# Kernel optimization log

Hardware: AMD Instinct MI355X
Metric: run time of the kernel (lower is better)

The kernel has to match this reference:

```python
import jax, jax.numpy as jnp
import numpy as np

EPS = 1e-5

def _conv3x3(x, w, b):
    # NCHW, OIHW, 3x3 stride 1 pad 1
    y = jax.lax.conv_general_dilated(x, w, window_strides=(1, 1),
                                     padding=((1, 1), (1, 1)),
                                     dimension_numbers=('NCHW', 'OIHW', 'NCHW'))
    return y + b[None, :, None, None]

def _pool_upsample(x, k):
    # adaptive avg pool to (H/k, W/k) then nearest block-upsample back
    B, C, H, W = x.shape
    p = x.reshape(B, C, H // k, k, W // k, k).mean(axis=(3, 5))
    return jnp.repeat(jnp.repeat(p, k, axis=2), k, axis=3)

def setup_inputs() -> dict:
    key = jax.random.key(0)
    ks = jax.random.split(key, 12)
    B, C, H, W = 32, 8, 300, 300
    d = {
        'x': jax.random.normal(ks[0], (B, C, H, W), jnp.float32),
        'w5': jax.random.normal(ks[1], (8, 16, 3, 3), jnp.float32) * 0.1,
        'b5': jnp.zeros((8,), jnp.float32),
        'w10': jax.random.normal(ks[2], (8, 16, 3, 3), jnp.float32) * 0.1,
        'b10': jnp.zeros((8,), jnp.float32),
        'w15': jax.random.normal(ks[3], (8, 16, 3, 3), jnp.float32) * 0.1,
        'b15': jnp.zeros((8,), jnp.float32),
        'gw': jax.random.normal(ks[4], (8, 24, 3, 3), jnp.float32) * 0.1,
        'gb': jnp.zeros((8,), jnp.float32),
        'mw': jax.random.normal(ks[5], (8, 24, 3, 3), jnp.float32) * 0.1,
        'mb': jnp.zeros((8,), jnp.float32),
        'gamma': jnp.ones((8,), jnp.float32),
        'beta': jnp.zeros((8,), jnp.float32),
    }
    return d

def reference(x, w5, b5, w10, b10, w15, b15, gw, gb, mw, mb, gamma, beta):
    up5 = _pool_upsample(x, 5)    # [B,8,300,300]
    up10 = _pool_upsample(x, 10)
    up15 = _pool_upsample(x, 15)
    c5 = _conv3x3(jnp.concatenate([x, up5], axis=1), w5, b5)
    c10 = _conv3x3(jnp.concatenate([x, up10], axis=1), w10, b10)
    c15 = _conv3x3(jnp.concatenate([x, up15], axis=1), w15, b15)
    g_in = jnp.concatenate([c5, c10, c15], axis=1)  # [B,24,H,W]
    # gated conv, activation=None: conv(g_in) * sigmoid(mask_conv(g_in))
    y = _conv3x3(g_in, gw, gb) * jax.nn.sigmoid(_conv3x3(g_in, mw, mb))
    # batch norm (training-mode batch stats, biased var, as torch default)
    mean = y.mean(axis=(0, 2, 3), keepdims=True)
    var = ((y - mean) ** 2).mean(axis=(0, 2, 3), keepdims=True)
    y = (y - mean) * jax.lax.rsqrt(var + EPS)
    return y * gamma[None, :, None, None] + beta[None, :, None, None]
```

## Files before the change

### kernel.cpp

```cpp
#include <hip/hip_runtime.h>
#include <math.h>

typedef __bf16 bfrag __attribute__((ext_vector_type(8)));
typedef __bf16 bf16x4 __attribute__((ext_vector_type(4)));
typedef __bf16 bf16x8 __attribute__((ext_vector_type(8)));
typedef float f32x4 __attribute__((ext_vector_type(4)));

#define BN 32
#define HH 300
#define WW 300
#define HW 90000
#define NPX (BN * HW)

#define GX 10
#define GY 19

#define P5I_BYTE_OFF   0
#define P10I_BYTE_OFF  1843200
#define P15I_BYTE_OFF  2304000
#define CWB_BYTE_OFF   2508800
#define GWB_BYTE_OFF   2524160
#define STAT_BYTE_OFF  2531328
#define SS_BYTE_OFF    2539520
#define XBF_BYTE_OFF   2539584
#define XBF_END        (XBF_BYTE_OFF + (size_t)NPX * 16)

__device__ __forceinline__ short f2bf(float f) {
    union { float f; unsigned u; } v;
    v.f = f;
    unsigned r = v.u + 0x7FFF + ((v.u >> 16) & 1);
    return (short)(r >> 16);
}

__device__ __forceinline__ float bf2f(unsigned short s) {
    union { unsigned u; float f; } v;
    v.u = ((unsigned)s) << 16;
    return v.f;
}

__global__ void k_setup(const float* __restrict__ w5, const float* __restrict__ w10,
                        const float* __restrict__ w15, const float* __restrict__ gw,
                        const float* __restrict__ mw, short* __restrict__ cBg,
                        short* __restrict__ gBg, double* __restrict__ stats) {
    int t = threadIdx.x;
    for (int idx = t; idx < 7680; idx += 256) {
        int s = idx / 2560, rem = idx % 2560;
        int n = rem / 160, r2 = rem % 160;
        int tap = r2 / 16, ci = r2 % 16;
        float v = 0.f;
        if (n < 8 && tap < 9) {
            const float* W = (s == 0) ? w5 : ((s == 1) ? w10 : w15);
            v = W[(n * 16 + ci) * 9 + tap];
        }
        cBg[idx] = f2bf(v);
    }
    for (int idx = t; idx < 3584; idx += 256) {
        int n = idx / 224, r2 = idx % 224;
        int blk = r2 / 8, cj = r2 % 8;
        float v = 0.f;
        if (blk < 27) {
            int tap = blk / 3, ci24 = (blk % 3) * 8 + cj;
            if (n < 8) v = gw[(n * 24 + ci24) * 9 + tap];
            else       v = mw[((n - 8) * 24 + ci24) * 9 + tap];
        }
        gBg[idx] = f2bf(v);
    }
    for (int idx = t; idx < 16 * 64; idx += 256) stats[idx] = 0.0;
}

__global__ void k_pool5(const float* __restrict__ x, unsigned short* __restrict__ p5i) {
    int id = blockIdx.x * 256 + threadIdx.x;
    int bc = id / 3600, cell = id % 3600;
    int b = bc >> 3, c = bc & 7;
    int pi = cell / 60, pj = cell % 60;
    const float* rp = x + (size_t)bc * HW + pi * 5 * WW + pj * 5;
    float s = 0.f;
#pragma unroll
    for (int u = 0; u < 5; u++)
#pragma unroll
        for (int v = 0; v < 5; v++) s += rp[u * WW + v];
    p5i[((size_t)b * 3600 + cell) * 8 + c] = (unsigned short)f2bf(s * 0.04f);
}

__global__ __launch_bounds__(256) void k_prep(const float* __restrict__ x,
                                              unsigned short* __restrict__ xbf,
                                              unsigned short* __restrict__ p5i) {
    __shared__ float tf[8][5][304];
    const int t = threadIdx.x;
    const int pi = blockIdx.x, b = blockIdx.y;
    for (int idx = t; idx < 3000; idx += 256) {
        int ch = idx / 375, rem = idx % 375;
        int r = rem / 75, j = rem % 75;
        float4 v = *(const float4*)&x[((size_t)(b * 8 + ch) * HH + pi * 5 + r) * WW + 4 * j];
        *(float4*)&tf[ch][r][4 * j] = v;
    }
    __syncthreads();
    for (int idx = t; idx < 1500; idx += 256) {
        int r = idx / 300, c = idx - r * 300;
        bf16x8 pk;
#pragma unroll
        for (int ch = 0; ch < 8; ch++) pk[ch] = (__bf16)tf[ch][r][c];
        *(bf16x8*)&xbf[((size_t)b * HW + (pi * 5 + r) * WW + c) * 8] = pk;
    }
    for (int idx = t; idx < 512; idx += 256) {
        int ch = idx >> 6, pj = idx & 63;
        if (pj < 60) {
            float s = 0.f;
#pragma unroll
            for (int u = 0; u < 5; u++)
#pragma unroll
                for (int v = 0; v < 5; v++) s += tf[ch][u][pj * 5 + v];
            p5i[((size_t)b * 3600 + pi * 60 + pj) * 8 + ch] = (unsigned short)f2bf(s * 0.04f);
        }
    }
}

__global__ void k_poolD(const unsigned short* __restrict__ p5i,
                        unsigned short* __restrict__ p10i,
                        unsigned short* __restrict__ p15i) {
    int id = blockIdx.x * 256 + threadIdx.x;
    if (id < 230400) {
        int bc = id / 900, cell = id % 900;
        int b = bc >> 3, c = bc & 7;
        int pi = cell / 30, pj = cell % 30;
        const unsigned short* base = p5i + ((size_t)b * 3600) * 8 + c;
        float s = bf2f(base[((2 * pi) * 60 + 2 * pj) * 8]) +
                  bf2f(base[((2 * pi) * 60 + 2 * pj + 1) * 8]) +
                  bf2f(base[((2 * pi + 1) * 60 + 2 * pj) * 8]) +
                  bf2f(base[((2 * pi + 1) * 60 + 2 * pj + 1) * 8]);
        p10i[((size_t)b * 900 + cell) * 8 + c] = (unsigned short)f2bf(s * 0.25f);
    } else if (id < 332800) {
        int id2 = id - 230400;
        int bc = id2 / 400, cell = id2 % 400;
        int b = bc >> 3, c = bc & 7;
        int pi = cell / 20, pj = cell % 20;
        const unsigned short* base = p5i + ((size_t)b * 3600) * 8 + c;
        float s = 0.f;
#pragma unroll
        for (int u = 0; u < 3; u++)
#pragma unroll
            for (int v = 0; v < 3; v++)
                s += bf2f(base[((3 * pi + u) * 60 + 3 * pj + v) * 8]);
        p15i[((size_t)b * 400 + cell) * 8 + c] = (unsigned short)f2bf(s * (1.f / 9.f));
    }
}

template <int K, int PW>
__device__ __forceinline__ void up_load(const unsigned short* __restrict__ pooled,
                                        int b, int r0, int c0, int t, uint4* v) {
#pragma unroll
    for (int it = 0; it < 3; it++) {
        int idx = t + 256 * it;
        uint4 val = {0u, 0u, 0u, 0u};
        if (idx < 720) {
            int i = idx / 36, j = idx - i * 36;
            int ra = r0 - 2 + i, ca = c0 - 2 + j;
            if (ra >= 0 && ra < HH && ca >= 0 && ca < WW) {
                int pi = (int)((unsigned)ra / K);
                int pj = (int)((unsigned)ca / K);
                val = *(const uint4*)&pooled[((size_t)b * (PW * PW) + pi * PW + pj) * 8];
            }
        }
        v[it] = val;
    }
}

__device__ __forceinline__ void up_store(short* xuU, int t, const uint4* v) {
#pragma unroll
    for (int it = 0; it < 3; it++) {
        int idx = t + 256 * it;
        if (idx < 720) *(uint4*)&xuU[idx * 8] = v[it];
    }
}

__device__ __forceinline__ void c_phase(const short* xuX, const short* xuU,
                                        short* cwS,
                                        const unsigned short* __restrict__ cBs,
                                        const float* __restrict__ bias, int s,
                                        int r0, int c0, int lane, int wid, bool edge) {
    const int n = lane & 15, quad = lane >> 4;
    const int qh = quad >> 1, ql = quad & 1;
    const short* xbase = ql ? xuU : xuX;
    bfrag wfr[5];
    int dpoff[5];
#pragma unroll
    for (int km = 0; km < 5; km++) {
        int tapw = km * 2 + qh;
        int tapa = (tapw > 8) ? 8 : tapw;
        wfr[km] = *(const bfrag*)&cBs[(n * 10 + tapw) * 16 + ql * 8];
        dpoff[km] = ((tapa / 3) * 36 + tapa % 3) * 8;
    }
    float bO[4];
#pragma unroll
    for (int r = 0; r < 4; r++) bO[r] = bias[(quad & 1) * 4 + r];

    for (int g = wid; g < 39; g += 4) {
        int px = g * 16 + n;
        if (px > 611) px = 611;
        int rp = (int)((unsigned)px / 34u);
        int cp = px - rp * 34;
        int pb = (rp * 36 + cp) * 8;
        f32x4 acc = {0.f, 0.f, 0.f, 0.f};
#pragma unroll
        for (int km = 0; km < 5; km++)
            acc = __builtin_amdgcn_mfma_f32_16x16x32_bf16(
                wfr[km], *(const bfrag*)&xbase[pb + dpoff[km]], acc, 0, 0, 0);
        if (quad < 2) {
            bf16x4 pk;
#pragma unroll
            for (int r = 0; r < 4; r++) pk[r] = (__bf16)(acc[r] + bO[r]);
            if (edge) {
                int ra = r0 - 1 + rp, ca = c0 - 1 + cp;
                if (ra < 0 || ra >= HH || ca < 0 || ca >= WW) {
#pragma unroll
                    for (int r = 0; r < 4; r++) pk[r] = (__bf16)0.f;
                }
            }
            *(bf16x4*)&cwS[px * 24 + s * 8 + quad * 4] = pk;
        }
    }
}

template <bool XBF>
__global__ __launch_bounds__(256, 3) void k_fused(
    const float* __restrict__ x, const unsigned short* __restrict__ xbf,
    const unsigned short* __restrict__ p5i, const unsigned short* __restrict__ p10i,
    const unsigned short* __restrict__ p15i,
    const unsigned short* __restrict__ cBg, const unsigned short* __restrict__ gBg,
    const float* __restrict__ b5, const float* __restrict__ b10, const float* __restrict__ b15,
    const float* __restrict__ gb, const float* __restrict__ mb,
    float* __restrict__ out, double* __restrict__ stats) {
    __shared__ __align__(16) short xuX[720 * 8];
    __shared__ __align__(16) short xuU[720 * 8];
    __shared__ __align__(16) short cwS[612 * 24];

    const int b = blockIdx.z;
    const int r0 = blockIdx.y * 16, c0 = blockIdx.x * 32;
    const int t = threadIdx.x, lane = t & 63, wid = t >> 6;
    const bool edge = (blockIdx.x == 0) | (blockIdx.x == GX - 1) |
                      (blockIdx.y == 0) | (blockIdx.y == GY - 1);

    uint4 upv[3];
    up_load<5, 60>(p5i, b, r0, c0, t, upv);

    if constexpr (XBF) {
        for (int it = 0; it < 3; it++) {
            int idx = t + 256 * it;
            if (idx < 720) {
                int i = idx / 36, j = idx - i * 36;
                int ra = r0 - 2 + i, ca = c0 - 2 + j;
                uint4 v = {0u, 0u, 0u, 0u};
                if (ra >= 0 && ra < HH && ca >= 0 && ca < WW)
                    v = *(const uint4*)&xbf[((size_t)b * HW + ra * WW + ca) * 8];
                *(uint4*)&xuX[idx * 8] = v;
            }
        }
    } else {
        for (int idx = t; idx < 1440; idx += 256) {
            int cp = idx / 360, rem = idx % 360;
            int i = rem / 18, jp = rem % 18;
            int j = 2 * jp;
            int ra = r0 - 2 + i, ca = c0 - 2 + j;
            float2 v0 = {0.f, 0.f}, v1 = {0.f, 0.f};
            if (ra >= 0 && ra < HH && ca >= 0 && ca <= WW - 2) {
                size_t base = ((size_t)(b * 8 + 2 * cp) * HH + ra) * WW + ca;
                v0 = *(const float2*)&x[base];
                v1 = *(const float2*)&x[base + HW];
            }
            unsigned pA = (unsigned short)f2bf(v0.x) | ((unsigned)(unsigned short)f2bf(v1.x) << 16);
            unsigned pB = (unsigned short)f2bf(v0.y) | ((unsigned)(unsigned short)f2bf(v1.y) << 16);
            int px = i * 36 + j;
            *(unsigned*)&xuX[px * 8 + 2 * cp] = pA;
            *(unsigned*)&xuX[(px + 1) * 8 + 2 * cp] = pB;
        }
    }
    up_store(xuU, t, upv);
    __syncthreads();

    c_phase(xuX, xuU, cwS, cBg, b5, 0, r0, c0, lane, wid, edge);
    up_load<10, 30>(p10i, b, r0, c0, t, upv);
    __syncthreads();
    up_store(xuU, t, upv);
    __syncthreads();

    c_phase(xuX, xuU, cwS, cBg + 2560, b10, 1, r0, c0, lane, wid, edge);
    up_load<15, 20>(p15i, b, r0, c0, t, upv);
    __syncthreads();
    up_store(xuU, t, upv);
    __syncthreads();

    c_phase(xuX, xuU, cwS, cBg + 5120, b15, 2, r0, c0, lane, wid, edge);
    __syncthreads();

    const int n = lane & 15, quad = lane >> 4;
    bfrag gfr[7];
    int goff[7];
#pragma unroll
    for (int km = 0; km < 7; km++) {
        int blkw = km * 4 + quad;
        int blka = (blkw > 26) ? 26 : blkw;
        gfr[km] = *(const bfrag*)&gBg[(n * 28 + blkw) * 8];
        int tap = blka / 3, cig = blka - tap * 3;
        goff[km] = ((tap / 3) * 34 + tap % 3) * 24 + cig * 8;
    }
    float gO[4], mO[4];
#pragma unroll
    for (int r = 0; r < 4; r++) {
        gO[r] = gb[(quad & 1) * 4 + r];
        mO[r] = mb[(quad & 1) * 4 + r];
    }
    float ls[4] = {0.f, 0.f, 0.f, 0.f}, ls2[4] = {0.f, 0.f, 0.f, 0.f};

    for (int g = wid; g < 32; g += 4) {
        int px = g * 16 + n;
        int rr = px >> 5, cc = px & 31;
        int off0 = (rr * 34 + cc) * 24;
        f32x4 acc = {0.f, 0.f, 0.f, 0.f};
#pragma unroll
        for (int km = 0; km < 7; km++)
            acc = __builtin_amdgcn_mfma_f32_16x16x32_bf16(
                gfr[km], *(const bfrag*)&cwS[off0 + goff[km]], acc, 0, 0, 0);
        int ra = r0 + rr, ca = c0 + cc;
        bool wr = !edge || (ra < HH && ca < WW);
#pragma unroll
        for (int reg = 0; reg < 4; reg++) {
            float other = __shfl_xor(acc[reg], 32);
            if (quad < 2 && wr) {
                float G = acc[reg] + gO[reg];
                float M = other + mO[reg];
                float y = G * __builtin_amdgcn_rcpf(1.f + __expf(-M));
                int ch = quad * 4 + reg;
                out[(size_t)(b * 8 + ch) * HW + ra * WW + ca] = y;
                ls[reg] += y;
                ls2[reg] += y * y;
            }
        }
    }
#pragma unroll
    for (int m = 1; m < 16; m <<= 1) {
#pragma unroll
        for (int r = 0; r < 4; r++) {
            ls[r] += __shfl_xor(ls[r], m);
            ls2[r] += __shfl_xor(ls2[r], m);
        }
    }
    if (n == 0 && quad < 2) {
        int hash = (blockIdx.x + GX * blockIdx.y + GX * GY * blockIdx.z) & 63;
#pragma unroll
        for (int r = 0; r < 4; r++) {
            atomicAdd(&stats[(quad * 4 + r) * 64 + hash], (double)ls[r]);
            atomicAdd(&stats[(8 + quad * 4 + r) * 64 + hash], (double)ls2[r]);
        }
    }
}

__global__ void k_stats(const double* __restrict__ stats, const float* __restrict__ gamma,
                        const float* __restrict__ beta, float* __restrict__ ss) {
    __shared__ double tot[16];
    int t = threadIdx.x;
    if (t < 16) {
        double s = 0.0;
        for (int i = 0; i < 64; i++) s += stats[t * 64 + i];
        tot[t] = s;
    }
    __syncthreads();
    if (t < 8) {
        double N = (double)NPX;
        double mean = tot[t] / N;
        double var = tot[8 + t] / N - mean * mean;
        double scale = (double)gamma[t] / sqrt(var + 1e-5);
        ss[t] = (float)scale;
        ss[8 + t] = (float)((double)beta[t] - mean * scale);
    }
}

__global__ void k_norm(float* __restrict__ out, const float* __restrict__ ss) {
    int i = blockIdx.x * 256 + threadIdx.x;
    if (i < (BN * 8 * HW) / 4) {
        int plane = (i * 4) / HW;
        int ch = plane & 7;
        float sc = ss[ch], sh = ss[8 + ch];
        float4* p = (float4*)out + i;
        float4 v = *p;
        v.x = v.x * sc + sh;
        v.y = v.y * sc + sh;
        v.z = v.z * sc + sh;
        v.w = v.w * sc + sh;
        *p = v;
    }
}

extern "C" void kernel_launch(void* const* d_in, const int* in_sizes, int n_in,
                              void* d_out, int out_size, void* d_ws, size_t ws_size,
                              hipStream_t stream) {
    const float* x = (const float*)d_in[0];
    const float* w5 = (const float*)d_in[1];
    const float* b5 = (const float*)d_in[2];
    const float* w10 = (const float*)d_in[3];
    const float* b10 = (const float*)d_in[4];
    const float* w15 = (const float*)d_in[5];
    const float* b15 = (const float*)d_in[6];
    const float* gw = (const float*)d_in[7];
    const float* gb = (const float*)d_in[8];
    const float* mw = (const float*)d_in[9];
    const float* mb = (const float*)d_in[10];
    const float* gamma = (const float*)d_in[11];
    const float* beta = (const float*)d_in[12];

    float* out = (float*)d_out;
    unsigned short* p5i = (unsigned short*)((char*)d_ws + P5I_BYTE_OFF);
    unsigned short* p10i = (unsigned short*)((char*)d_ws + P10I_BYTE_OFF);
    unsigned short* p15i = (unsigned short*)((char*)d_ws + P15I_BYTE_OFF);
    short* cBg = (short*)((char*)d_ws + CWB_BYTE_OFF);
    short* gBg = (short*)((char*)d_ws + GWB_BYTE_OFF);
    double* stats = (double*)((char*)d_ws + STAT_BYTE_OFF);
    float* ss = (float*)((char*)d_ws + SS_BYTE_OFF);
    unsigned short* xbf = (unsigned short*)((char*)d_ws + XBF_BYTE_OFF);

    const bool use_xbf = (ws_size >= XBF_END);

    k_setup<<<1, 256, 0, stream>>>(w5, w10, w15, gw, mw, cBg, gBg, stats);
    if (use_xbf) {
        k_prep<<<dim3(60, 32), 256, 0, stream>>>(x, xbf, p5i);
    } else {
        k_pool5<<<3600, 256, 0, stream>>>(x, p5i);
    }
    k_poolD<<<1300, 256, 0, stream>>>(p5i, p10i, p15i);
    dim3 grid(GX, GY, BN);
    if (use_xbf) {
        k_fused<true><<<grid, 256, 0, stream>>>(x, xbf, p5i, p10i, p15i,
                                                (const unsigned short*)cBg, (const unsigned short*)gBg,
                                                b5, b10, b15, gb, mb, out, stats);
    } else {
        k_fused<false><<<grid, 256, 0, stream>>>(x, xbf, p5i, p10i, p15i,
                                                 (const unsigned short*)cBg, (const unsigned short*)gBg,
                                                 b5, b10, b15, gb, mb, out, stats);
    }
    k_stats<<<1, 64, 0, stream>>>(stats, gamma, beta, ss);
    k_norm<<<(BN * 8 * HW / 4 + 255) / 256, 256, 0, stream>>>(out, ss);
}
```

Baseline: 390.7 us.

## Split prep into xbf conversion and pool kernels, planar conv LDS layout

Replaces the fused prep kernel with a simple per-pixel fp32-to-bf16 channel-interleave kernel that also performs weight setup, removing one launch. A separate kernel then computes 5x5 pooling from the bf16 buffer. The intermediate conv outputs in LDS move from an interleaved 24-channel layout to three planar 8-channel buffers, which is meant to cut bank conflicts. The gated epilogue now splits the sigmoid and gate work across half-waves before the shuffle, and the stats reduction is parallelized. Pooling from bf16 instead of fp32 changes rounding slightly and adds an extra read pass over xbf.

```diff
diff --git a/kernel.cpp b/kernel.cpp
--- a/kernel.cpp
+++ b/kernel.cpp
@@ -14,6 +14,9 @@
 
 #define GX 10
 #define GY 19
+#define CPX 612
+#define XPX 720
+#define CWSTRIDE 4896
 
 #define P5I_BYTE_OFF   0
 #define P10I_BYTE_OFF  1843200
@@ -38,12 +41,16 @@
     return v.f;
 }
 
-__global__ void k_setup(const float* __restrict__ w5, const float* __restrict__ w10,
-                        const float* __restrict__ w15, const float* __restrict__ gw,
-                        const float* __restrict__ mw, short* __restrict__ cBg,
-                        short* __restrict__ gBg, double* __restrict__ stats) {
-    int t = threadIdx.x;
-    for (int idx = t; idx < 7680; idx += 256) {
+__device__ __forceinline__ void setup_body(int gid, int gstride,
+                                           const float* __restrict__ w5,
+                                           const float* __restrict__ w10,
+                                           const float* __restrict__ w15,
+                                           const float* __restrict__ gw,
+                                           const float* __restrict__ mw,
+                                           short* __restrict__ cBg,
+                                           short* __restrict__ gBg,
+                                           double* __restrict__ stats) {
+    for (int idx = gid; idx < 7680; idx += gstride) {
         int s = idx / 2560, rem = idx % 2560;
         int n = rem / 160, r2 = rem % 160;
         int tap = r2 / 16, ci = r2 % 16;
@@ -54,7 +61,7 @@
         }
         cBg[idx] = f2bf(v);
     }
-    for (int idx = t; idx < 3584; idx += 256) {
+    for (int idx = gid; idx < 3584; idx += gstride) {
         int n = idx / 224, r2 = idx % 224;
         int blk = r2 / 8, cj = r2 % 8;
         float v = 0.f;
@@ -65,7 +72,39 @@
         }
         gBg[idx] = f2bf(v);
     }
-    for (int idx = t; idx < 16 * 64; idx += 256) stats[idx] = 0.0;
+    for (int idx = gid; idx < 16 * 64; idx += gstride) stats[idx] = 0.0;
+}
+
+__global__ void k_setup(const float* __restrict__ w5, const float* __restrict__ w10,
+                        const float* __restrict__ w15, const float* __restrict__ gw,
+                        const float* __restrict__ mw, short* __restrict__ cBg,
+                        short* __restrict__ gBg, double* __restrict__ stats) {
+    setup_body(threadIdx.x, 256, w5, w10, w15, gw, mw, cBg, gBg, stats);
+}
+
+__global__ __launch_bounds__(256) void k_xbf(const float* __restrict__ x,
+                                             unsigned short* __restrict__ xbf,
+                                             const float* __restrict__ w5,
+                                             const float* __restrict__ w10,
+                                             const float* __restrict__ w15,
+                                             const float* __restrict__ gw,
+                                             const float* __restrict__ mw,
+                                             short* __restrict__ cBg,
+                                             short* __restrict__ gBg,
+                                             double* __restrict__ stats) {
+    const int b = blockIdx.y;
+    const int px = blockIdx.x * 256 + threadIdx.x;
+    if (px < HW) {
+        const float* xp = x + (size_t)b * 8 * HW + px;
+        bf16x8 pk;
+#pragma unroll
+        for (int ch = 0; ch < 8; ch++) pk[ch] = (__bf16)xp[(size_t)ch * HW];
+        *(bf16x8*)&xbf[((size_t)b * HW + px) * 8] = pk;
+    }
+    if (blockIdx.y == 0 && blockIdx.x < 16) {
+        int gid = blockIdx.x * 256 + threadIdx.x;
+        setup_body(gid, 4096, w5, w10, w15, gw, mw, cBg, gBg, stats);
+    }
 }
 
 __global__ void k_pool5(const float* __restrict__ x, unsigned short* __restrict__ p5i) {
@@ -82,37 +121,25 @@
     p5i[((size_t)b * 3600 + cell) * 8 + c] = (unsigned short)f2bf(s * 0.04f);
 }
 
-__global__ __launch_bounds__(256) void k_prep(const float* __restrict__ x,
-                                              unsigned short* __restrict__ xbf,
-                                              unsigned short* __restrict__ p5i) {
-    __shared__ float tf[8][5][304];
-    const int t = threadIdx.x;
-    const int pi = blockIdx.x, b = blockIdx.y;
-    for (int idx = t; idx < 3000; idx += 256) {
-        int ch = idx / 375, rem = idx % 375;
-        int r = rem / 75, j = rem % 75;
-        float4 v = *(const float4*)&x[((size_t)(b * 8 + ch) * HH + pi * 5 + r) * WW + 4 * j];
-        *(float4*)&tf[ch][r][4 * j] = v;
-    }
-    __syncthreads();
-    for (int idx = t; idx < 1500; idx += 256) {
-        int r = idx / 300, c = idx - r * 300;
-        bf16x8 pk;
-#pragma unroll
-        for (int ch = 0; ch < 8; ch++) pk[ch] = (__bf16)tf[ch][r][c];
-        *(bf16x8*)&xbf[((size_t)b * HW + (pi * 5 + r) * WW + c) * 8] = pk;
-    }
-    for (int idx = t; idx < 512; idx += 256) {
-        int ch = idx >> 6, pj = idx & 63;
-        if (pj < 60) {
-            float s = 0.f;
-#pragma unroll
-            for (int u = 0; u < 5; u++)
-#pragma unroll
-                for (int v = 0; v < 5; v++) s += tf[ch][u][pj * 5 + v];
-            p5i[((size_t)b * 3600 + pi * 60 + pj) * 8 + ch] = (unsigned short)f2bf(s * 0.04f);
-        }
-    }
+__global__ __launch_bounds__(256) void k_pool5b(const unsigned short* __restrict__ xbf,
+                                                unsigned short* __restrict__ p5i) {
+    int id = blockIdx.x * 256 + threadIdx.x;
+    int b = id / 3600, cell = id % 3600;
+    int pi = cell / 60, pj = cell % 60;
+    const unsigned short* base = xbf + ((size_t)b * HW + pi * 5 * WW + pj * 5) * 8;
+    float s[8] = {0.f, 0.f, 0.f, 0.f, 0.f, 0.f, 0.f, 0.f};
+#pragma unroll
+    for (int u = 0; u < 5; u++)
+#pragma unroll
+        for (int v = 0; v < 5; v++) {
+            bf16x8 vv = *(const bf16x8*)&base[(u * WW + v) * 8];
+#pragma unroll
+            for (int ch = 0; ch < 8; ch++) s[ch] += (float)vv[ch];
+        }
+    bf16x8 pk;
+#pragma unroll
+    for (int ch = 0; ch < 8; ch++) pk[ch] = (__bf16)(s[ch] * 0.04f);
+    *(bf16x8*)&p5i[((size_t)b * 3600 + cell) * 8] = pk;
 }
 
 __global__ void k_poolD(const unsigned short* __restrict__ p5i,
@@ -152,7 +179,7 @@
     for (int it = 0; it < 3; it++) {
         int idx = t + 256 * it;
         uint4 val = {0u, 0u, 0u, 0u};
-        if (idx < 720) {
+        if (idx < XPX) {
             int i = idx / 36, j = idx - i * 36;
             int ra = r0 - 2 + i, ca = c0 - 2 + j;
             if (ra >= 0 && ra < HH && ca >= 0 && ca < WW) {
@@ -169,14 +196,14 @@
 #pragma unroll
     for (int it = 0; it < 3; it++) {
         int idx = t + 256 * it;
-        if (idx < 720) *(uint4*)&xuU[idx * 8] = v[it];
+        if (idx < XPX) *(uint4*)&xuU[idx * 8] = v[it];
     }
 }
 
 __device__ __forceinline__ void c_phase(const short* xuX, const short* xuU,
-                                        short* cwS,
+                                        short* cwP,
                                         const unsigned short* __restrict__ cBs,
-                                        const float* __restrict__ bias, int s,
+                                        const float* __restrict__ bias,
                                         int r0, int c0, int lane, int wid, bool edge) {
     const int n = lane & 15, quad = lane >> 4;
     const int qh = quad >> 1, ql = quad & 1;
@@ -216,7 +243,7 @@
                     for (int r = 0; r < 4; r++) pk[r] = (__bf16)0.f;
                 }
             }
-            *(bf16x4*)&cwS[px * 24 + s * 8 + quad * 4] = pk;
+            *(bf16x4*)&cwP[px * 8 + quad * 4] = pk;
         }
     }
 }
@@ -230,9 +257,9 @@
     const float* __restrict__ b5, const float* __restrict__ b10, const float* __restrict__ b15,
     const float* __restrict__ gb, const float* __restrict__ mb,
     float* __restrict__ out, double* __restrict__ stats) {
-    __shared__ __align__(16) short xuX[720 * 8];
-    __shared__ __align__(16) short xuU[720 * 8];
-    __shared__ __align__(16) short cwS[612 * 24];
+    __shared__ __align__(16) short xuX[XPX * 8];
+    __shared__ __align__(16) short xuU[XPX * 8];
+    __shared__ __align__(16) short cwS[3 * CWSTRIDE];
 
     const int b = blockIdx.z;
     const int r0 = blockIdx.y * 16, c0 = blockIdx.x * 32;
@@ -244,9 +271,10 @@
     up_load<5, 60>(p5i, b, r0, c0, t, upv);
 
     if constexpr (XBF) {
+#pragma unroll
         for (int it = 0; it < 3; it++) {
             int idx = t + 256 * it;
-            if (idx < 720) {
+            if (idx < XPX) {
                 int i = idx / 36, j = idx - i * 36;
                 int ra = r0 - 2 + i, ca = c0 - 2 + j;
                 uint4 v = {0u, 0u, 0u, 0u};
@@ -277,19 +305,19 @@
     up_store(xuU, t, upv);
     __syncthreads();
 
-    c_phase(xuX, xuU, cwS, cBg, b5, 0, r0, c0, lane, wid, edge);
+    c_phase(xuX, xuU, cwS, cBg, b5, r0, c0, lane, wid, edge);
     up_load<10, 30>(p10i, b, r0, c0, t, upv);
     __syncthreads();
     up_store(xuU, t, upv);
     __syncthreads();
 
-    c_phase(xuX, xuU, cwS, cBg + 2560, b10, 1, r0, c0, lane, wid, edge);
+    c_phase(xuX, xuU, cwS + CWSTRIDE, cBg + 2560, b10, r0, c0, lane, wid, edge);
     up_load<15, 20>(p15i, b, r0, c0, t, upv);
     __syncthreads();
     up_store(xuU, t, upv);
     __syncthreads();
 
-    c_phase(xuX, xuU, cwS, cBg + 5120, b15, 2, r0, c0, lane, wid, edge);
+    c_phase(xuX, xuU, cwS + 2 * CWSTRIDE, cBg + 5120, b15, r0, c0, lane, wid, edge);
     __syncthreads();
 
     const int n = lane & 15, quad = lane >> 4;
@@ -301,7 +329,7 @@
         int blka = (blkw > 26) ? 26 : blkw;
         gfr[km] = *(const bfrag*)&gBg[(n * 28 + blkw) * 8];
         int tap = blka / 3, cig = blka - tap * 3;
-        goff[km] = ((tap / 3) * 34 + tap % 3) * 24 + cig * 8;
+        goff[km] = cig * CWSTRIDE + ((tap / 3) * 34 + tap % 3) * 8;
     }
     float gO[4], mO[4];
 #pragma unroll
@@ -314,7 +342,7 @@
     for (int g = wid; g < 32; g += 4) {
         int px = g * 16 + n;
         int rr = px >> 5, cc = px & 31;
-        int off0 = (rr * 34 + cc) * 24;
+        int off0 = (rr * 34 + cc) * 8;
         f32x4 acc = {0.f, 0.f, 0.f, 0.f};
 #pragma unroll
         for (int km = 0; km < 7; km++)
@@ -324,13 +352,14 @@
         bool wr = !edge || (ra < HH && ca < WW);
 #pragma unroll
         for (int reg = 0; reg < 4; reg++) {
-            float other = __shfl_xor(acc[reg], 32);
+            float val;
+            if (quad < 2) val = acc[reg] + gO[reg];
+            else          val = __builtin_amdgcn_rcpf(1.f + __expf(-(acc[reg] + mO[reg])));
+            float other = __shfl_xor(val, 32);
             if (quad < 2 && wr) {
-                float G = acc[reg] + gO[reg];
-                float M = other + mO[reg];
-                float y = G * __builtin_amdgcn_rcpf(1.f + __expf(-M));
+                float y = val * other;
                 int ch = quad * 4 + reg;
-                out[(size_t)(b * 8 + ch) * HW + ra * WW + ca] = y;
+                out[(size_t)(b * 8 + ch) * HW + (size_t)ra * WW + ca] = y;
                 ls[reg] += y;
                 ls2[reg] += y * y;
             }
@@ -356,18 +385,24 @@
 
 __global__ void k_stats(const double* __restrict__ stats, const float* __restrict__ gamma,
                         const float* __restrict__ beta, float* __restrict__ ss) {
-    __shared__ double tot[16];
+    __shared__ double red[16][16];
     int t = threadIdx.x;
+    int row = t >> 4, col = t & 15;
+    double s = stats[row * 64 + col] + stats[row * 64 + col + 16] +
+               stats[row * 64 + col + 32] + stats[row * 64 + col + 48];
+    red[row][col] = s;
+    __syncthreads();
     if (t < 16) {
-        double s = 0.0;
-        for (int i = 0; i < 64; i++) s += stats[t * 64 + i];
-        tot[t] = s;
+        double tot = 0.0;
+#pragma unroll
+        for (int i = 0; i < 16; i++) tot += red[t][i];
+        red[t][0] = tot;
     }
     __syncthreads();
     if (t < 8) {
         double N = (double)NPX;
-        double mean = tot[t] / N;
-        double var = tot[8 + t] / N - mean * mean;
+        double mean = red[t][0] / N;
+        double var = red[8 + t][0] / N - mean * mean;
         double scale = (double)gamma[t] / sqrt(var + 1e-5);
         ss[t] = (float)scale;
         ss[8 + t] = (float)((double)beta[t] - mean * scale);
@@ -419,23 +454,23 @@
 
     const bool use_xbf = (ws_size >= XBF_END);
 
-    k_setup<<<1, 256, 0, stream>>>(w5, w10, w15, gw, mw, cBg, gBg, stats);
-    if (use_xbf) {
-        k_prep<<<dim3(60, 32), 256, 0, stream>>>(x, xbf, p5i);
-    } else {
-        k_pool5<<<3600, 256, 0, stream>>>(x, p5i);
-    }
-    k_poolD<<<1300, 256, 0, stream>>>(p5i, p10i, p15i);
     dim3 grid(GX, GY, BN);
     if (use_xbf) {
+        k_xbf<<<dim3(352, 32), 256, 0, stream>>>(x, xbf, w5, w10, w15, gw, mw,
+                                                 cBg, gBg, stats);
+        k_pool5b<<<450, 256, 0, stream>>>(xbf, p5i);
+        k_poolD<<<1300, 256, 0, stream>>>(p5i, p10i, p15i);
         k_fused<true><<<grid, 256, 0, stream>>>(x, xbf, p5i, p10i, p15i,
                                                 (const unsigned short*)cBg, (const unsigned short*)gBg,
                                                 b5, b10, b15, gb, mb, out, stats);
     } else {
+        k_setup<<<1, 256, 0, stream>>>(w5, w10, w15, gw, mw, cBg, gBg, stats);
+        k_pool5<<<3600, 256, 0, stream>>>(x, p5i);
+        k_poolD<<<1300, 256, 0, stream>>>(p5i, p10i, p15i);
         k_fused<false><<<grid, 256, 0, stream>>>(x, xbf, p5i, p10i, p15i,
                                                  (const unsigned short*)cBg, (const unsigned short*)gBg,
                                                  b5, b10, b15, gb, mb, out, stats);
     }
-    k_stats<<<1, 64, 0, stream>>>(stats, gamma, beta, ss);
+    k_stats<<<1, 256, 0, stream>>>(stats, gamma, beta, ss);
     k_norm<<<(BN * 8 * HW / 4 + 255) / 256, 256, 0, stream>>>(out, ss);
 }
```

New measurement: 387.4 us. No clear change (-0.8%).
